# Kernel tuning notes

Measured on AMD Instinct MI355X. Metric: run time of the kernel, lower is better.

## Reference

```python
import jax, jax.numpy as jnp
import numpy as np

B = 8192          # num_envs
OPT = 16          # num options
SHARED = 22       # shared_state_size (hardcoded in module)
UNIQ = 8          # unique_state_size (hardcoded in module)
MIN_DUR, MAX_DUR = 0.1, 0.5  # const.gait_net.valid_swing_duration_range


def _w(k, o, i):
    return jax.random.normal(k, (o, i), jnp.float32) * (1.0 / np.sqrt(i))


def setup_inputs() -> dict:
    key = jax.random.key(0)
    ks = jax.random.split(key, 20)
    obs = jax.random.normal(ks[0], (B, SHARED + OPT * UNIQ), jnp.float32)
    flag = jax.random.uniform(ks[1], (B, OPT)) < 0.25
    u = obs[:, SHARED:].reshape(B, OPT, UNIQ)
    u = u.at[:, :, 0].set(jnp.where(flag, 1.0, u[:, :, 0]))
    obs = jnp.concatenate([obs[:, :SHARED], u.reshape(B, OPT * UNIQ)], axis=1)
    return {
        "obs": obs,
        "sw1": _w(ks[2], 256, 22), "sb1": jnp.zeros((256,), jnp.float32),
        "sw2": _w(ks[3], 256, 256), "sb2": jnp.zeros((256,), jnp.float32),
        "uw1": _w(ks[4], 128, 8), "ub1": jnp.zeros((128,), jnp.float32),
        "uw2": _w(ks[5], 128, 128), "ub2": jnp.zeros((128,), jnp.float32),
        "no_op_embedding": jax.random.normal(ks[6], (128,), jnp.float32),
        "tw1": _w(ks[7], 512, 384), "tb1": jnp.zeros((512,), jnp.float32),
        "tw2": _w(ks[8], 256, 512), "tb2": jnp.zeros((256,), jnp.float32),
        "vw": _w(ks[9], 1, 256), "vb": jnp.zeros((1,), jnp.float32),
        "dw": _w(ks[10], 1, 256), "db": jnp.zeros((1,), jnp.float32),
    }


def reference(obs, sw1, sb1, sw2, sb2, uw1, ub1, uw2, ub2, no_op_embedding,
              tw1, tb1, tw2, tb2, vw, vb, dw, db):
    relu = jax.nn.relu
    shared = obs[:, :SHARED]                               # [B, 22]
    uniq = obs[:, SHARED:].reshape(B, OPT, UNIQ)           # [B, OPT, 8]
    # shared encoder (22 -> 256 -> 256, relu output)
    se = relu(relu(shared @ sw1.T + sb1) @ sw2.T + sb2)    # [B, 256]
    # unique encoder applied to all options at once (8 -> 128 -> 128)
    ue = relu(relu(uniq @ uw1.T + ub1) @ uw2.T + ub2)      # [B, OPT, 128]
    no_op = uniq[:, :, 0] == 1.0                           # [B, OPT]
    ue = jnp.where(no_op[..., None], no_op_embedding, ue)
    trunk_in = jnp.concatenate(
        [jnp.broadcast_to(se[:, None, :], (B, OPT, se.shape[-1])), ue], axis=-1)
    t = relu(relu(trunk_in @ tw1.T + tb1) @ tw2.T + tb2)   # [B, OPT, 256]
    logits = (t @ vw.T + vb).squeeze(-1)                   # [B, OPT]
    duration = jax.nn.sigmoid((t @ dw.T + db).squeeze(-1)) * (MAX_DUR - MIN_DUR) + MIN_DUR
    return logits, duration
```

## Files before the change

### kernel.cpp

```cpp
#include <hip/hip_runtime.h>
#include <stdint.h>


static constexpr int B_ = 8192;

typedef __attribute__((ext_vector_type(8))) short bf16x8;
typedef __attribute__((ext_vector_type(4))) float f32x4;

__device__ __forceinline__ float u2f(uint16_t u) {
    union { uint32_t i; float f; } c; c.i = (uint32_t)u << 16; return c.f;
}
__device__ __forceinline__ uint16_t f2u(float f) {
    __bf16 b = (__bf16)f;
    return __builtin_bit_cast(uint16_t, b);
}
__device__ __forceinline__ ushort4 pack4(float a, float b, float c, float d) {
    ushort4 o;
    o.x = f2u(a); o.y = f2u(b); o.z = f2u(c); o.w = f2u(d);
    return o;
}

static constexpr size_t WCSE   = 0;
static constexpr size_t WTW1SE = 4194304;
static constexpr size_t WTW1UE = WTW1SE + 131072;
static constexpr size_t WTW2   = WTW1UE + 65536;
static constexpr size_t WUW2   = WTW2 + 131072;
static constexpr size_t WSW2   = WUW2 + 16384;
static constexpr size_t WUW1B  = WSW2 + 65536;

__global__ __launch_bounds__(256) void k_conv(
    const float* __restrict__ tw1, const float* __restrict__ tw2,
    const float* __restrict__ uw2, const float* __restrict__ sw2,
    const float* __restrict__ uw1, uint16_t* __restrict__ ws)
{
    int i4 = blockIdx.x * 256 + threadIdx.x;
    if (i4 >= 102400) {
        int q = i4 - 102400;
        int n = q >> 3, k0 = (q & 7) * 4;
        ushort4 o = {0, 0, 0, 0};
        if (k0 < 8) {
            float4 v = *reinterpret_cast<const float4*>(uw1 + n * 8 + k0);
            o.x = f2u(v.x); o.y = f2u(v.y); o.z = f2u(v.z); o.w = f2u(v.w);
        }
        *reinterpret_cast<ushort4*>(ws + WUW1B + n * 32 + k0) = o;
        return;
    }
    const float* src; size_t dst;
    if (i4 < 32768) {
        int g = i4 * 4, n = g >> 8, k = g & 255;
        src = tw1 + (size_t)n * 384 + k;
        dst = WTW1SE + (size_t)g;
    } else if (i4 < 49152) {
        int q = i4 - 32768, n = q >> 5, w = q & 31;
        src = tw1 + (size_t)n * 384 + 256 + w * 4;
        dst = WTW1UE + (size_t)n * 128 + w * 4;
    } else if (i4 < 81920) {
        int q = (i4 - 49152) * 4;
        src = tw2 + q; dst = WTW2 + q;
    } else if (i4 < 86016) {
        int q = (i4 - 81920) * 4;
        src = uw2 + q; dst = WUW2 + q;
    } else {
        int q = (i4 - 86016) * 4;
        src = sw2 + q; dst = WSW2 + q;
    }
    float4 v = *reinterpret_cast<const float4*>(src);
    ushort4 o;
    o.x = f2u(v.x); o.y = f2u(v.y); o.z = f2u(v.z); o.w = f2u(v.w);
    *reinterpret_cast<ushort4*>(ws + dst) = o;
}

__global__ __launch_bounds__(512) void k_cse(
    const float* __restrict__ obs,
    const float* __restrict__ sw1, const float* __restrict__ sb1,
    const float* __restrict__ sb2, const float* __restrict__ tb1,
    uint16_t* __restrict__ ws)
{
    __shared__ float xs[16][24];
    __shared__ uint16_t h1s[16 * 264];
    __shared__ uint16_t seL[16 * 264];
    const int t = threadIdx.x;
    const int b0 = blockIdx.x * 16;
    const uint16_t* sw2b   = ws + WSW2;
    const uint16_t* tw1seb = ws + WTW1SE;

    if (t < 352) {
        int e = t / 22, c = t - e * 22;
        xs[e][c] = obs[(size_t)(b0 + e) * 150 + c];
    }
    __syncthreads();
    {
        const int n = t & 255;
        float w[22];
        #pragma unroll
        for (int k = 0; k < 22; ++k) w[k] = sw1[n * 22 + k];
        const float bias = sb1[n];
        #pragma unroll
        for (int ii = 0; ii < 8; ++ii) {
            int e = (t >> 8) * 8 + ii;
            float a = bias;
            #pragma unroll
            for (int k = 0; k < 22; ++k) a += w[k] * xs[e][k];
            h1s[e * 264 + n] = f2u(fmaxf(a, 0.f));
        }
    }
    __syncthreads();
    const int wv = t >> 6, lane = t & 63, quad = lane >> 4, l16 = lane & 15;
    {
        f32x4 acc[2];
        #pragma unroll
        for (int nt = 0; nt < 2; ++nt) {
            float bv = sb2[wv * 32 + nt * 16 + l16];
            acc[nt] = {bv, bv, bv, bv};
        }
        const uint16_t* bb = sw2b + (size_t)(wv * 32 + l16) * 256 + quad * 8;
        bf16x8 bc[2], bn[2];
        bc[0] = *reinterpret_cast<const bf16x8*>(bb);
        bc[1] = *reinterpret_cast<const bf16x8*>(bb + 4096);
        #pragma unroll
        for (int kk = 0; kk < 8; ++kk) {
            if (kk < 7) {
                bn[0] = *reinterpret_cast<const bf16x8*>(bb + (kk + 1) * 32);
                bn[1] = *reinterpret_cast<const bf16x8*>(bb + 4096 + (kk + 1) * 32);
            }
            bf16x8 af = *reinterpret_cast<const bf16x8*>(
                &h1s[l16 * 264 + kk * 32 + quad * 8]);
            #pragma unroll
            for (int nt = 0; nt < 2; ++nt)
                acc[nt] = __builtin_amdgcn_mfma_f32_16x16x32_bf16(
                    af, bc[nt], acc[nt], 0, 0, 0);
            bc[0] = bn[0]; bc[1] = bn[1];
        }
        #pragma unroll
        for (int nt = 0; nt < 2; ++nt)
            #pragma unroll
            for (int r = 0; r < 4; ++r)
                seL[(quad * 4 + r) * 264 + wv * 32 + nt * 16 + l16] =
                    f2u(fmaxf(acc[nt][r], 0.f));
    }
    __syncthreads();
    {
        f32x4 acc[4];
        #pragma unroll
        for (int nt = 0; nt < 4; ++nt) {
            float bv = tb1[wv * 64 + nt * 16 + l16];
            acc[nt] = {bv, bv, bv, bv};
        }
        const uint16_t* bb = tw1seb + (size_t)(wv * 64 + l16) * 256 + quad * 8;
        bf16x8 bc[4], bn[4];
        #pragma unroll
        for (int nt = 0; nt < 4; ++nt)
            bc[nt] = *reinterpret_cast<const bf16x8*>(bb + nt * 4096);
        #pragma unroll
        for (int kk = 0; kk < 8; ++kk) {
            if (kk < 7) {
                #pragma unroll
                for (int nt = 0; nt < 4; ++nt)
                    bn[nt] = *reinterpret_cast<const bf16x8*>(
                        bb + nt * 4096 + (kk + 1) * 32);
            }
            bf16x8 af = *reinterpret_cast<const bf16x8*>(
                &seL[l16 * 264 + kk * 32 + quad * 8]);
            #pragma unroll
            for (int nt = 0; nt < 4; ++nt)
                acc[nt] = __builtin_amdgcn_mfma_f32_16x16x32_bf16(
                    af, bc[nt], acc[nt], 0, 0, 0);
            #pragma unroll
            for (int nt = 0; nt < 4; ++nt) bc[nt] = bn[nt];
        }
        #pragma unroll
        for (int nt = 0; nt < 4; ++nt)
            #pragma unroll
            for (int r = 0; r < 4; ++r)
                ws[WCSE + (size_t)(b0 + quad * 4 + r) * 512 +
                   wv * 64 + nt * 16 + l16] = f2u(acc[nt][r]);
    }
}

static constexpr int UQB_OFF  = 0;
static constexpr int NOOP_OFF = 5120;
static constexpr int CSE_OFF  = 5376;
static constexpr int H1U_OFF  = 9472;
static constexpr int UET_OFF  = 26880;
static constexpr int H1T_OFF  = 44288;
static constexpr int SMEM_SZ  = 78080;

__global__ __launch_bounds__(512, 4) void k_main(
    const float* __restrict__ obs,
    const float* __restrict__ ub1,
    const float* __restrict__ ub2, const float* __restrict__ emb,
    const float* __restrict__ tb2,
    const float* __restrict__ vw,  const float* __restrict__ vb,
    const float* __restrict__ dw,  const float* __restrict__ db,
    const uint16_t* __restrict__ wsb,
    float* __restrict__ out)
{
    __shared__ __align__(16) char smem[SMEM_SZ];
    uint16_t* uqb   = (uint16_t*)(smem + UQB_OFF);
    float*    noopf = (float*)(smem + NOOP_OFF);
    uint16_t* cseL  = (uint16_t*)(smem + CSE_OFF);
    uint16_t* h1u   = (uint16_t*)(smem + H1U_OFF);
    uint16_t* uet   = (uint16_t*)(smem + UET_OFF);
    uint16_t* h1t   = (uint16_t*)(smem + H1T_OFF);
    uint16_t* t2    = h1t;

    const int t    = threadIdx.x;
    const int wv   = t >> 6;
    const int lane = t & 63;
    const int quad = lane >> 4;
    const int l16  = lane & 15;
    const int b0   = blockIdx.x * 4;

    const uint16_t* csep  = wsb + WCSE;
    const uint16_t* tw1ue = wsb + WTW1UE;
    const uint16_t* tw2b  = wsb + WTW2;
    const uint16_t* uw2b  = wsb + WUW2;
    const uint16_t* uw1b  = wsb + WUW1B;

    {
        int r = t >> 3, q = t & 7;
        int e = r >> 4, o = r & 15;
        ushort4 ov = {0, 0, 0, 0};
        if (q < 2) {
            const float2* sp = reinterpret_cast<const float2*>(
                &obs[(size_t)(b0 + e) * 150 + 22 + o * 8 + q * 4]);
            float2 a = sp[0], b = sp[1];
            ov.x = f2u(a.x); ov.y = f2u(a.y); ov.z = f2u(b.x); ov.w = f2u(b.y);
        }
        *reinterpret_cast<ushort4*>(&uqb[r * 40 + q * 4]) = ov;
        #pragma unroll
        for (int ii = 0; ii < 2; ++ii) {
            int i = t + ii * 512;
            int ee = i >> 8, cc = i & 255;
            ((uint32_t*)cseL)[ee * 256 + cc] =
                ((const uint32_t*)(csep + (size_t)(b0 + ee) * 512))[cc];
        }
        if (t < 64) {
            int ee = t >> 4, oo = t & 15;
            noopf[t] = (obs[(size_t)(b0 + ee) * 150 + 22 + oo * 8] == 1.0f) ? 1.0f : 0.0f;
        }
    }
    __syncthreads();

    {
        float4 bv4 = *reinterpret_cast<const float4*>(&ub1[wv * 16 + quad * 4]);
        f32x4 acc[4];
        #pragma unroll
        for (int mt = 0; mt < 4; ++mt) acc[mt] = {bv4.x, bv4.y, bv4.z, bv4.w};
        bf16x8 wf = *reinterpret_cast<const bf16x8*>(
            &uw1b[(wv * 16 + l16) * 32 + quad * 8]);
        #pragma unroll
        for (int mt = 0; mt < 4; ++mt) {
            bf16x8 xf = *reinterpret_cast<const bf16x8*>(
                &uqb[(mt * 16 + l16) * 40 + quad * 8]);
            acc[mt] = __builtin_amdgcn_mfma_f32_16x16x32_bf16(wf, xf, acc[mt], 0, 0, 0);
        }
        #pragma unroll
        for (int mt = 0; mt < 4; ++mt) {
            ushort4 o = pack4(fmaxf(acc[mt][0], 0.f), fmaxf(acc[mt][1], 0.f),
                              fmaxf(acc[mt][2], 0.f), fmaxf(acc[mt][3], 0.f));
            *reinterpret_cast<ushort4*>(
                &h1u[(mt * 16 + l16) * 136 + wv * 16 + quad * 4]) = o;
        }
    }
    __syncthreads();

    {
        float4 bv4 = *reinterpret_cast<const float4*>(&ub2[wv * 16 + quad * 4]);
        float4 ev4 = *reinterpret_cast<const float4*>(&emb[wv * 16 + quad * 4]);
        f32x4 acc[4];
        #pragma unroll
        for (int mt = 0; mt < 4; ++mt) acc[mt] = {bv4.x, bv4.y, bv4.z, bv4.w};
        #pragma unroll
        for (int kk = 0; kk < 4; ++kk) {
            bf16x8 wf = *reinterpret_cast<const bf16x8*>(
                &uw2b[(size_t)(wv * 16 + l16) * 128 + kk * 32 + quad * 8]);
            #pragma unroll
            for (int mt = 0; mt < 4; ++mt) {
                bf16x8 xf = *reinterpret_cast<const bf16x8*>(
                    &h1u[(mt * 16 + l16) * 136 + kk * 32 + quad * 8]);
                acc[mt] = __builtin_amdgcn_mfma_f32_16x16x32_bf16(wf, xf, acc[mt], 0, 0, 0);
            }
        }
        #pragma unroll
        for (int mt = 0; mt < 4; ++mt) {
            bool noop = (noopf[mt * 16 + l16] != 0.0f);
            ushort4 o = pack4(noop ? ev4.x : fmaxf(acc[mt][0], 0.f),
                              noop ? ev4.y : fmaxf(acc[mt][1], 0.f),
                              noop ? ev4.z : fmaxf(acc[mt][2], 0.f),
                              noop ? ev4.w : fmaxf(acc[mt][3], 0.f));
            *reinterpret_cast<ushort4*>(
                &uet[(mt * 16 + l16) * 136 + wv * 16 + quad * 4]) = o;
        }
    }
    __syncthreads();

    f32x4 acc2[4][2];
    #pragma unroll
    for (int nt = 0; nt < 2; ++nt) {
        float4 bv4 = *reinterpret_cast<const float4*>(
            &tb2[wv * 32 + nt * 16 + quad * 4]);
        #pragma unroll
        for (int mt = 0; mt < 4; ++mt) acc2[mt][nt] = {bv4.x, bv4.y, bv4.z, bv4.w};
    }

    #pragma unroll
    for (int nc = 0; nc < 2; ++nc) {
        {
            f32x4 acc1[4][2];
            #pragma unroll
            for (int nt = 0; nt < 2; ++nt) {
                int n0 = nc * 256 + wv * 32 + nt * 16 + quad * 4;
                #pragma unroll
                for (int mt = 0; mt < 4; ++mt) {
                    ushort4 cv = *reinterpret_cast<const ushort4*>(
                        &cseL[mt * 512 + n0]);
                    acc1[mt][nt] = {u2f(cv.x), u2f(cv.y), u2f(cv.z), u2f(cv.w)};
                }
            }
            const uint16_t* bb = tw1ue + (size_t)(nc * 256 + wv * 32 + l16) * 128
                                 + quad * 8;
            bf16x8 bc[2], bn[2];
            bc[0] = *reinterpret_cast<const bf16x8*>(bb);
            bc[1] = *reinterpret_cast<const bf16x8*>(bb + 2048);
            #pragma unroll
            for (int kk = 0; kk < 4; ++kk) {
                if (kk < 3) {
                    bn[0] = *reinterpret_cast<const bf16x8*>(bb + (kk + 1) * 32);
                    bn[1] = *reinterpret_cast<const bf16x8*>(bb + 2048 + (kk + 1) * 32);
                }
                bf16x8 af[4];
                #pragma unroll
                for (int mt = 0; mt < 4; ++mt)
                    af[mt] = *reinterpret_cast<const bf16x8*>(
                        &uet[(mt * 16 + l16) * 136 + kk * 32 + quad * 8]);
                #pragma unroll
                for (int mt = 0; mt < 4; ++mt)
                    #pragma unroll
                    for (int nt = 0; nt < 2; ++nt)
                        acc1[mt][nt] = __builtin_amdgcn_mfma_f32_16x16x32_bf16(
                            bc[nt], af[mt], acc1[mt][nt], 0, 0, 0);
                bc[0] = bn[0]; bc[1] = bn[1];
            }
            #pragma unroll
            for (int mt = 0; mt < 4; ++mt)
                #pragma unroll
                for (int nt = 0; nt < 2; ++nt) {
                    ushort4 o = pack4(fmaxf(acc1[mt][nt][0], 0.f),
                                      fmaxf(acc1[mt][nt][1], 0.f),
                                      fmaxf(acc1[mt][nt][2], 0.f),
                                      fmaxf(acc1[mt][nt][3], 0.f));
                    *reinterpret_cast<ushort4*>(
                        &h1t[(mt * 16 + l16) * 264 + wv * 32 + nt * 16 + quad * 4]) = o;
                }
        }
        __syncthreads();
        {
            const uint16_t* cb = tw2b + (size_t)(wv * 32 + l16) * 512 + nc * 256
                                 + quad * 8;
            bf16x8 cc[2], cn[2];
            cc[0] = *reinterpret_cast<const bf16x8*>(cb);
            cc[1] = *reinterpret_cast<const bf16x8*>(cb + 8192);
            #pragma unroll
            for (int k2 = 0; k2 < 8; ++k2) {
                if (k2 < 7) {
                    cn[0] = *reinterpret_cast<const bf16x8*>(cb + (k2 + 1) * 32);
                    cn[1] = *reinterpret_cast<const bf16x8*>(cb + 8192 + (k2 + 1) * 32);
                }
                bf16x8 af[4];
                #pragma unroll
                for (int mt = 0; mt < 4; ++mt)
                    af[mt] = *reinterpret_cast<const bf16x8*>(
                        &h1t[(mt * 16 + l16) * 264 + k2 * 32 + quad * 8]);
                #pragma unroll
                for (int mt = 0; mt < 4; ++mt)
                    #pragma unroll
                    for (int nt = 0; nt < 2; ++nt)
                        acc2[mt][nt] = __builtin_amdgcn_mfma_f32_16x16x32_bf16(
                            cc[nt], af[mt], acc2[mt][nt], 0, 0, 0);
                cc[0] = cn[0]; cc[1] = cn[1];
            }
        }
        if (nc == 0) __syncthreads();
    }
    __syncthreads();
    #pragma unroll
    for (int mt = 0; mt < 4; ++mt)
        #pragma unroll
        for (int nt = 0; nt < 2; ++nt) {
            ushort4 o = pack4(fmaxf(acc2[mt][nt][0], 0.f),
                              fmaxf(acc2[mt][nt][1], 0.f),
                              fmaxf(acc2[mt][nt][2], 0.f),
                              fmaxf(acc2[mt][nt][3], 0.f));
            *reinterpret_cast<ushort4*>(
                &t2[(mt * 16 + l16) * 264 + wv * 32 + nt * 16 + quad * 4]) = o;
        }
    __syncthreads();

    {
        float vwf[4], dwf[4];
        #pragma unroll
        for (int j = 0; j < 4; ++j) {
            vwf[j] = vw[lane + 64 * j];
            dwf[j] = dw[lane + 64 * j];
        }
        const float vbf = vb[0], dbf = db[0];
        #pragma unroll
        for (int rr = 0; rr < 8; ++rr) {
            int row = wv * 8 + rr;
            float sv = 0.f, sd = 0.f;
            #pragma unroll
            for (int j = 0; j < 4; ++j) {
                float tv = u2f(t2[row * 264 + lane + 64 * j]);
                sv += tv * vwf[j];
                sd += tv * dwf[j];
            }
            #pragma unroll
            for (int off = 32; off > 0; off >>= 1) {
                sv += __shfl_down(sv, off);
                sd += __shfl_down(sd, off);
            }
            if (lane == 0) {
                int g = blockIdx.x * 64 + row;
                out[g] = sv + vbf;
                float z = sd + dbf;
                float sig = 1.f / (1.f + __expf(-z));
                out[B_ * 16 + g] = sig * 0.4f + 0.1f;
            }
        }
    }
}

extern "C" void kernel_launch(void* const* d_in, const int* in_sizes, int n_in,
                              void* d_out, int out_size, void* d_ws, size_t ws_size,
                              hipStream_t stream) {
    const float* obs = (const float*)d_in[0];
    const float* sw1 = (const float*)d_in[1];
    const float* sb1 = (const float*)d_in[2];
    const float* sw2 = (const float*)d_in[3];
    const float* sb2 = (const float*)d_in[4];
    const float* uw1 = (const float*)d_in[5];
    const float* ub1 = (const float*)d_in[6];
    const float* uw2 = (const float*)d_in[7];
    const float* ub2 = (const float*)d_in[8];
    const float* emb = (const float*)d_in[9];
    const float* tw1 = (const float*)d_in[10];
    const float* tb1 = (const float*)d_in[11];
    const float* tw2 = (const float*)d_in[12];
    const float* tb2 = (const float*)d_in[13];
    const float* vw  = (const float*)d_in[14];
    const float* vb  = (const float*)d_in[15];
    const float* dw  = (const float*)d_in[16];
    const float* db  = (const float*)d_in[17];

    uint16_t* wsb = (uint16_t*)d_ws;

    k_conv<<<404, 256, 0, stream>>>(tw1, tw2, uw2, sw2, uw1, wsb);
    k_cse<<<512, 512, 0, stream>>>(obs, sw1, sb1, sb2, tb1, wsb);
    k_main<<<B_ / 4, 512, 0, stream>>>(obs, ub1, ub2, emb, tb2,
                                       vw, vb, dw, db, wsb, (float*)d_out);
}
```

Baseline: 234.2 us.

## Fuse value/duration heads into MFMA epilogue and prefetch shared encoding into registers

The trunk output heads are now computed directly from the MFMA accumulators. Each lane takes partial dot products with the value and duration weights, reduces across quads with xor shuffles, and sums the per-wave partials through a small shared-memory buffer. This removes the bf16 write of the second trunk layer to LDS, an extra barrier, and the per-row shuffle reductions. The load of the precomputed shared encoding is also issued early into registers and stored to LDS after the unique-encoder stage, so its global latency overlaps compute. The head sums now use fp32 activations instead of rounding through bf16, which slightly changes numerics.

```diff
diff --git a/kernel.cpp b/kernel.cpp
--- a/kernel.cpp
+++ b/kernel.cpp
@@ -202,7 +202,7 @@
     uint16_t* h1u   = (uint16_t*)(smem + H1U_OFF);
     uint16_t* uet   = (uint16_t*)(smem + UET_OFF);
     uint16_t* h1t   = (uint16_t*)(smem + H1T_OFF);
-    uint16_t* t2    = h1t;
+    float*    hred  = (float*)(smem + H1T_OFF);
 
     const int t    = threadIdx.x;
     const int wv   = t >> 6;
@@ -217,6 +217,7 @@
     const uint16_t* uw2b  = wsb + WUW2;
     const uint16_t* uw1b  = wsb + WUW1B;
 
+    uint32_t cse_r0, cse_r1;
     {
         int r = t >> 3, q = t & 7;
         int e = r >> 4, o = r & 15;
@@ -228,13 +229,9 @@
             ov.x = f2u(a.x); ov.y = f2u(a.y); ov.z = f2u(b.x); ov.w = f2u(b.y);
         }
         *reinterpret_cast<ushort4*>(&uqb[r * 40 + q * 4]) = ov;
-        #pragma unroll
-        for (int ii = 0; ii < 2; ++ii) {
-            int i = t + ii * 512;
-            int ee = i >> 8, cc = i & 255;
-            ((uint32_t*)cseL)[ee * 256 + cc] =
-                ((const uint32_t*)(csep + (size_t)(b0 + ee) * 512))[cc];
-        }
+        const uint32_t* cp = (const uint32_t*)(csep + (size_t)b0 * 512);
+        cse_r0 = cp[t];
+        cse_r1 = cp[t + 512];
         if (t < 64) {
             int ee = t >> 4, oo = t & 15;
             noopf[t] = (obs[(size_t)(b0 + ee) * 150 + 22 + oo * 8] == 1.0f) ? 1.0f : 0.0f;
@@ -292,6 +289,8 @@
             *reinterpret_cast<ushort4*>(
                 &uet[(mt * 16 + l16) * 136 + wv * 16 + quad * 4]) = o;
         }
+        ((uint32_t*)cseL)[t] = cse_r0;
+        ((uint32_t*)cseL)[t + 512] = cse_r1;
     }
     __syncthreads();
 
@@ -384,49 +383,54 @@
         if (nc == 0) __syncthreads();
     }
     __syncthreads();
-    #pragma unroll
-    for (int mt = 0; mt < 4; ++mt)
+
+    {
+        float svr[4] = {0.f, 0.f, 0.f, 0.f};
+        float sdr[4] = {0.f, 0.f, 0.f, 0.f};
         #pragma unroll
         for (int nt = 0; nt < 2; ++nt) {
-            ushort4 o = pack4(fmaxf(acc2[mt][nt][0], 0.f),
-                              fmaxf(acc2[mt][nt][1], 0.f),
-                              fmaxf(acc2[mt][nt][2], 0.f),
-                              fmaxf(acc2[mt][nt][3], 0.f));
-            *reinterpret_cast<ushort4*>(
-                &t2[(mt * 16 + l16) * 264 + wv * 32 + nt * 16 + quad * 4]) = o;
-        }
-    __syncthreads();
-
-    {
-        float vwf[4], dwf[4];
-        #pragma unroll
-        for (int j = 0; j < 4; ++j) {
-            vwf[j] = vw[lane + 64 * j];
-            dwf[j] = dw[lane + 64 * j];
-        }
-        const float vbf = vb[0], dbf = db[0];
-        #pragma unroll
-        for (int rr = 0; rr < 8; ++rr) {
-            int row = wv * 8 + rr;
-            float sv = 0.f, sd = 0.f;
-            #pragma unroll
-            for (int j = 0; j < 4; ++j) {
-                float tv = u2f(t2[row * 264 + lane + 64 * j]);
-                sv += tv * vwf[j];
-                sd += tv * dwf[j];
-            }
-            #pragma unroll
-            for (int off = 32; off > 0; off >>= 1) {
-                sv += __shfl_down(sv, off);
-                sd += __shfl_down(sd, off);
-            }
-            if (lane == 0) {
-                int g = blockIdx.x * 64 + row;
-                out[g] = sv + vbf;
-                float z = sd + dbf;
-                float sig = 1.f / (1.f + __expf(-z));
-                out[B_ * 16 + g] = sig * 0.4f + 0.1f;
-            }
+            float4 vw4 = *reinterpret_cast<const float4*>(
+                &vw[wv * 32 + nt * 16 + quad * 4]);
+            float4 dw4 = *reinterpret_cast<const float4*>(
+                &dw[wv * 32 + nt * 16 + quad * 4]);
+            #pragma unroll
+            for (int mt = 0; mt < 4; ++mt) {
+                float t0 = fmaxf(acc2[mt][nt][0], 0.f);
+                float t1 = fmaxf(acc2[mt][nt][1], 0.f);
+                float t2 = fmaxf(acc2[mt][nt][2], 0.f);
+                float t3 = fmaxf(acc2[mt][nt][3], 0.f);
+                svr[mt] += t0 * vw4.x + t1 * vw4.y + t2 * vw4.z + t3 * vw4.w;
+                sdr[mt] += t0 * dw4.x + t1 * dw4.y + t2 * dw4.z + t3 * dw4.w;
+            }
+        }
+        #pragma unroll
+        for (int mt = 0; mt < 4; ++mt) {
+            svr[mt] += __shfl_xor(svr[mt], 16);
+            svr[mt] += __shfl_xor(svr[mt], 32);
+            sdr[mt] += __shfl_xor(sdr[mt], 16);
+            sdr[mt] += __shfl_xor(sdr[mt], 32);
+        }
+        if (quad == 0) {
+            #pragma unroll
+            for (int mt = 0; mt < 4; ++mt) {
+                int row = mt * 16 + l16;
+                hred[(row * 2 + 0) * 8 + wv] = svr[mt];
+                hred[(row * 2 + 1) * 8 + wv] = sdr[mt];
+            }
+        }
+    }
+    __syncthreads();
+    if (t < 128) {
+        const float* p = &hred[t * 8];
+        float s = p[0] + p[1] + p[2] + p[3] + p[4] + p[5] + p[6] + p[7];
+        int row = t >> 1;
+        int g = blockIdx.x * 64 + row;
+        if ((t & 1) == 0) {
+            out[g] = s + vb[0];
+        } else {
+            float z = s + db[0];
+            float sig = 1.f / (1.f + __expf(-z));
+            out[B_ * 16 + g] = sig * 0.4f + 0.1f;
         }
     }
 }
```

Result: faster. 224.4 us (-4.2%).
